# Performance work log

Measured on AMD Instinct MI355X. Metric: run time of the kernel, lower is better.

The kernel has to match this reference:

```python
import jax, jax.numpy as jnp
import numpy as np

N = 25000   # nodes
M = 150000  # edges
D = 512     # d_Embedding
H = 8       # heads
DK = 64     # per-head key dim
DV = 64     # per-head value dim


def setup_inputs() -> dict:
    key = jax.random.key(0)
    ks = jax.random.split(key, 8)
    x = jax.random.normal(ks[0], (N, D), jnp.float32)
    edge_index = jax.random.randint(ks[1], (2, M), 0, N).astype(jnp.int32)
    s_in = 1.0 / np.sqrt(D).astype(np.float32)   # fan-in scaling like nn.Linear init
    s_ff = 1.0 / np.sqrt(H * DV).astype(np.float32)
    Wk = jax.random.normal(ks[2], (D, H * DK), jnp.float32) * s_in
    Wq = jax.random.normal(ks[3], (D, H * DK), jnp.float32) * s_in
    Wv = jax.random.normal(ks[4], (D, H * DV), jnp.float32) * s_in
    Wff = jax.random.normal(ks[5], (H * DV, D), jnp.float32) * s_ff
    bk = jnp.zeros((H * DK,), jnp.float32)
    bq = jnp.zeros((H * DK,), jnp.float32)
    bv = jnp.zeros((H * DV,), jnp.float32)
    bff = jnp.zeros((D,), jnp.float32)
    return {"x": x, "edge_index": edge_index, "Wk": Wk, "bk": bk,
            "Wq": Wq, "bq": bq, "Wv": Wv, "bv": bv, "Wff": Wff, "bff": bff}


def reference(x, edge_index, Wk, bk, Wq, bq, Wv, bv, Wff, bff):
    # Q/K/V projections with per-head reshape (make_heads)
    K = (x @ Wk + bk).reshape(-1, H, DK)
    Q = (x @ Wq + bq).reshape(-1, H, DK)
    V = (x @ Wv + bv).reshape(-1, H, DV)
    senders, receivers = edge_index[0], edge_index[1]
    # edge scores: (M, H)
    att = jnp.einsum('mhd,mhd->mh', Q[receivers], K[senders]) / np.sqrt(DK).astype(np.float32)
    att = jnp.exp(att + 3.0 - att.max())  # global-max-shifted exp, as in source
    # normalize by sum of incoming strengths per receiver node (segment softmax denom)
    ssum = jax.ops.segment_sum(att, receivers, num_segments=N)  # (N, H)
    denom = ssum[receivers]
    att = jnp.where(denom == 0, 0.0, att / jnp.where(denom == 0, 1.0, denom))
    # weighted message + scatter-add aggregate: (N, H, DV)
    msg = att[..., None] * V[senders]
    agg = jax.ops.segment_sum(msg, receivers, num_segments=N)
    # aggregate_heads: Linear over concatenated heads
    return agg.reshape(-1, H * DV) @ Wff + bff
```

## Files before the change

kernel.cpp:

```cpp
#include <hip/hip_runtime.h>
#include <hip/hip_bf16.h>

#define DMODEL 512

typedef __attribute__((ext_vector_type(8))) short bf16x8;
typedef __attribute__((ext_vector_type(4))) float f32x4;

__device__ inline void gload_lds16(const void* g, void* s) {
  __builtin_amdgcn_global_load_lds((const __attribute__((address_space(1))) void*)g,
                                   (__attribute__((address_space(3))) void*)s, 16, 0, 0);
}

__device__ inline float bflo(unsigned u) {
  union { float f; unsigned u; } c; c.u = u << 16; return c.f;
}
__device__ inline float bfhi(unsigned u) {
  union { float f; unsigned u; } c; c.u = u & 0xffff0000u; return c.f;
}

template <bool OUT_BF16, int NT>
__global__ __launch_bounds__(512, 2)
void gemm_quad(const __hip_bfloat16* __restrict__ Ap,
               const __hip_bfloat16* __restrict__ Wp,
               const float* __restrict__ bias, void* __restrict__ Cv,
               int Nrows, int ncols) {
  __shared__ __align__(16) short sA[32768];
  const int tid = threadIdx.x;
  const int lane = tid & 63, w = tid >> 6;
  const int q = blockIdx.x;
  const __hip_bfloat16* Aq = Ap + (size_t)q * 32768;

#pragma unroll
  for (int i = 0; i < 8; ++i)
    gload_lds16(Aq + (size_t)(i * 512 + tid) * 8, &sA[(i * 512 + tid) * 8]);
  __syncthreads();

  const int l15 = lane & 15, lq = lane >> 4;

#pragma unroll 1
  for (int gs = 0; gs < NT / 4; ++gs) {
    const int ntb = w * NT + gs * 4;
    const __hip_bfloat16* Wb = Wp + (size_t)ntb * 16 * 512 + lane * 8;
    f32x4 acc[4][4] = {};
    bf16x8 b_cur[4], b_nxt[4];
#pragma unroll
    for (int n = 0; n < 4; ++n)
      b_cur[n] = *(const bf16x8*)(Wb + (size_t)(n * 16) * 512);

#pragma unroll 1
    for (int c = 0; c < 16; ++c) {
      if (c < 15) {
#pragma unroll
        for (int n = 0; n < 4; ++n)
          b_nxt[n] = *(const bf16x8*)(Wb + (size_t)(n * 16 + c + 1) * 512);
      }
#pragma unroll
      for (int m = 0; m < 4; ++m) {
        bf16x8 af = *(const bf16x8*)&sA[(m * 16 + c) * 512 + lane * 8];
#pragma unroll
        for (int n = 0; n < 4; ++n)
          acc[m][n] = __builtin_amdgcn_mfma_f32_16x16x32_bf16(af, b_cur[n], acc[m][n], 0, 0, 0);
      }
      if (c < 15) {
#pragma unroll
        for (int n = 0; n < 4; ++n) b_cur[n] = b_nxt[n];
      }
    }

#pragma unroll
    for (int m = 0; m < 4; ++m) {
      int rowb = q * 64 + m * 16;
#pragma unroll
      for (int n = 0; n < 4; ++n) {
        int col = (ntb + n) * 16 + l15;
        float bv = bias[col];
#pragma unroll
        for (int i = 0; i < 4; ++i) {
          int row = rowb + lq * 4 + i;
          if (row < Nrows) {
            float v = acc[m][n][i] + bv;
            if (OUT_BF16)
              ((__hip_bfloat16*)Cv)[(size_t)row * ncols + col] = __float2bfloat16(v);
            else
              ((float*)Cv)[(size_t)row * ncols + col] = v;
          }
        }
      }
    }
  }
}

__global__ void cvtp_kernel(const float* __restrict__ x, __hip_bfloat16* __restrict__ xp,
                            int Nrows, int NpadRows) {
  int tid = blockIdx.x * 256 + threadIdx.x;
  int r = tid >> 6, kb = tid & 63;
  if (r >= NpadRows) return;
  int t = r >> 4, c = kb >> 2, qq = kb & 3, lp = qq * 16 + (r & 15);
  __hip_bfloat16* dst = xp + (size_t)t * 8192 + c * 512 + lp * 8;
  union { ushort4 u[2]; __hip_bfloat16 h[8]; } o;
#pragma unroll
  for (int j = 0; j < 8; ++j) o.h[j] = __float2bfloat16(0.f);
  if (r < Nrows) {
    float4 v0 = *(const float4*)(x + (size_t)r * DMODEL + kb * 8);
    float4 v1 = *(const float4*)(x + (size_t)r * DMODEL + kb * 8 + 4);
    o.h[0] = __float2bfloat16(v0.x); o.h[1] = __float2bfloat16(v0.y);
    o.h[2] = __float2bfloat16(v0.z); o.h[3] = __float2bfloat16(v0.w);
    o.h[4] = __float2bfloat16(v1.x); o.h[5] = __float2bfloat16(v1.y);
    o.h[6] = __float2bfloat16(v1.z); o.h[7] = __float2bfloat16(v1.w);
  }
  *(ushort4*)dst = o.u[0];
  *(ushort4*)(dst + 4) = o.u[1];
}

__global__ __launch_bounds__(256)
void wp_kernel(const float* __restrict__ Wk, const float* __restrict__ Wq,
               const float* __restrict__ Wv, const float* __restrict__ Wff,
               __hip_bfloat16* __restrict__ Wp_qkv, __hip_bfloat16* __restrict__ Wp_ff) {
  int c = blockIdx.x;
  int S = blockIdx.y;
  const float* W; __hip_bfloat16* dst;
  if (S < 8)       { W = Wk;  dst = Wp_qkv + (size_t)S * 32768; }
  else if (S < 16) { W = Wq;  dst = Wp_qkv + (size_t)S * 32768; }
  else if (S < 24) { W = Wv;  dst = Wp_qkv + (size_t)S * 32768; }
  else             { W = Wff; dst = Wp_ff + (size_t)(S - 24) * 32768; }
  int colbase = (S & 7) * 64;
  __shared__ float tile[32][64];
  for (int idx = threadIdx.x; idx < 2048; idx += 256) {
    int r = idx >> 6, col = idx & 63;
    tile[r][col] = W[(size_t)(c * 32 + r) * DMODEL + colbase + col];
  }
  __syncthreads();
  int n = threadIdx.x >> 6, l = threadIdx.x & 63;
  union { ushort4 u[2]; __hip_bfloat16 h[8]; } o;
#pragma unroll
  for (int j = 0; j < 8; ++j)
    o.h[j] = __float2bfloat16(tile[(l >> 4) * 8 + j][n * 16 + (l & 15)]);
  __hip_bfloat16* p = dst + ((size_t)(n * 16 + c) * 64 + l) * 8;
  *(ushort4*)p = o.u[0];
  *(ushort4*)(p + 4) = o.u[1];
}

__global__ void bias_kernel(const float* __restrict__ bk, const float* __restrict__ bq,
                            const float* __restrict__ bv, float* __restrict__ o) {
  int i = blockIdx.x * 256 + threadIdx.x;
  if (i < 512) o[i] = bk[i];
  else if (i < 1024) o[i] = bq[i - 512];
  else if (i < 1536) o[i] = bv[i - 1024];
}

__global__ void hist_kernel(const int* __restrict__ recv, int* __restrict__ deg, int M_) {
  int m = blockIdx.x * 256 + threadIdx.x;
  if (m < M_) atomicAdd(&deg[recv[m]], 1);
}

__global__ __launch_bounds__(256)
void scan_block(const int* __restrict__ deg, int* __restrict__ offs,
                int* __restrict__ bsum, int n) {
  __shared__ int sd[256];
  const int t = threadIdx.x;
  const int base = blockIdx.x * 1024;
  int v[4], s = 0;
#pragma unroll
  for (int j = 0; j < 4; ++j) {
    int idx = base + t * 4 + j;
    v[j] = (idx < n) ? deg[idx] : 0;
    s += v[j];
  }
  sd[t] = s;
  __syncthreads();
  for (int off = 1; off < 256; off <<= 1) {
    int x = (t >= off) ? sd[t - off] : 0;
    __syncthreads();
    sd[t] += x;
    __syncthreads();
  }
  int run = sd[t] - s;
#pragma unroll
  for (int j = 0; j < 4; ++j) {
    int idx = base + t * 4 + j;
    if (idx < n) offs[idx] = run;
    run += v[j];
  }
  if (t == 255) bsum[blockIdx.x] = sd[255];
}

__global__ void scan_mid(const int* __restrict__ bsum, int* __restrict__ bbase,
                         int nb, int* __restrict__ offs, int n) {
  int t = threadIdx.x;
  int x = (t < nb) ? bsum[t] : 0;
  int v = x;
  for (int off = 1; off < 64; off <<= 1) {
    int y = __shfl_up(v, off);
    if (t >= off) v += y;
  }
  if (t < nb) bbase[t] = v - x;
  if (t == nb - 1) offs[n] = v;
}

__global__ void scan_add(int* __restrict__ offs, const int* __restrict__ bbase,
                         int* __restrict__ cursor, int n) {
  int i = blockIdx.x * 256 + threadIdx.x;
  if (i < n) {
    int o = offs[i] + bbase[i >> 10];
    offs[i] = o;
    cursor[i] = o;
  }
}

__global__ void fill_kernel(const int* __restrict__ senders, const int* __restrict__ recv,
                            int* __restrict__ cursor, int* __restrict__ sidx, int M_) {
  int m = blockIdx.x * 256 + threadIdx.x;
  if (m < M_) {
    int pos = atomicAdd(&cursor[recv[m]], 1);
    sidx[pos] = senders[m];
  }
}

__global__ __launch_bounds__(256)
void attn_kernel(const __hip_bfloat16* __restrict__ QKV, const int* __restrict__ sidx,
                 const int* __restrict__ offs, __hip_bfloat16* __restrict__ aggp, int n) {
  const int lane = threadIdx.x & 63;
  const int wid  = threadIdx.x >> 6;
  const int r = blockIdx.x * 4 + wid;
  if (r >= n) return;
  const int start = offs[r];
  const int end   = offs[r + 1];

  uint4 qr = *(const uint4*)(QKV + (size_t)r * 1536 + 512 + lane * 8);
  float q[8] = {bflo(qr.x), bfhi(qr.x), bflo(qr.y), bfhi(qr.y),
                bflo(qr.z), bfhi(qr.z), bflo(qr.w), bfhi(qr.w)};

  float ssum = 0.f;
  float acc[8] = {};
  int e = start;
  for (; e + 2 <= end; e += 2) {
    int s0 = sidx[e], s1 = sidx[e + 1];
    const __hip_bfloat16* p0 = QKV + (size_t)s0 * 1536 + lane * 8;
    const __hip_bfloat16* p1 = QKV + (size_t)s1 * 1536 + lane * 8;
    uint4 k0 = *(const uint4*)p0;
    uint4 v0 = *(const uint4*)(p0 + 1024);
    uint4 k1 = *(const uint4*)p1;
    uint4 v1 = *(const uint4*)(p1 + 1024);
    float d0 = q[0] * bflo(k0.x) + q[1] * bfhi(k0.x) + q[2] * bflo(k0.y) + q[3] * bfhi(k0.y)
             + q[4] * bflo(k0.z) + q[5] * bfhi(k0.z) + q[6] * bflo(k0.w) + q[7] * bfhi(k0.w);
    float d1 = q[0] * bflo(k1.x) + q[1] * bfhi(k1.x) + q[2] * bflo(k1.y) + q[3] * bfhi(k1.y)
             + q[4] * bflo(k1.z) + q[5] * bfhi(k1.z) + q[6] * bflo(k1.w) + q[7] * bfhi(k1.w);
    d0 += __shfl_xor(d0, 1); d1 += __shfl_xor(d1, 1);
    d0 += __shfl_xor(d0, 2); d1 += __shfl_xor(d1, 2);
    d0 += __shfl_xor(d0, 4); d1 += __shfl_xor(d1, 4);
    float w0 = expf(d0 * 0.125f), w1 = expf(d1 * 0.125f);
    ssum += w0 + w1;
    acc[0] += w0 * bflo(v0.x) + w1 * bflo(v1.x);
    acc[1] += w0 * bfhi(v0.x) + w1 * bfhi(v1.x);
    acc[2] += w0 * bflo(v0.y) + w1 * bflo(v1.y);
    acc[3] += w0 * bfhi(v0.y) + w1 * bfhi(v1.y);
    acc[4] += w0 * bflo(v0.z) + w1 * bflo(v1.z);
    acc[5] += w0 * bfhi(v0.z) + w1 * bfhi(v1.z);
    acc[6] += w0 * bflo(v0.w) + w1 * bflo(v1.w);
    acc[7] += w0 * bfhi(v0.w) + w1 * bfhi(v1.w);
  }
  if (e < end) {
    int s0 = sidx[e];
    const __hip_bfloat16* p0 = QKV + (size_t)s0 * 1536 + lane * 8;
    uint4 k0 = *(const uint4*)p0;
    uint4 v0 = *(const uint4*)(p0 + 1024);
    float d0 = q[0] * bflo(k0.x) + q[1] * bfhi(k0.x) + q[2] * bflo(k0.y) + q[3] * bfhi(k0.y)
             + q[4] * bflo(k0.z) + q[5] * bfhi(k0.z) + q[6] * bflo(k0.w) + q[7] * bfhi(k0.w);
    d0 += __shfl_xor(d0, 1);
    d0 += __shfl_xor(d0, 2);
    d0 += __shfl_xor(d0, 4);
    float w0 = expf(d0 * 0.125f);
    ssum += w0;
    acc[0] += w0 * bflo(v0.x); acc[1] += w0 * bfhi(v0.x);
    acc[2] += w0 * bflo(v0.y); acc[3] += w0 * bfhi(v0.y);
    acc[4] += w0 * bflo(v0.z); acc[5] += w0 * bfhi(v0.z);
    acc[6] += w0 * bflo(v0.w); acc[7] += w0 * bfhi(v0.w);
  }
  const float inv = (end > start) ? 1.0f / ssum : 0.f;
  union { ushort4 u[2]; __hip_bfloat16 h[8]; } o;
#pragma unroll
  for (int j = 0; j < 8; ++j) o.h[j] = __float2bfloat16(acc[j] * inv);
  int t = r >> 4, c = lane >> 2, qq = lane & 3, lp = qq * 16 + (r & 15);
  __hip_bfloat16* dst = aggp + (size_t)t * 8192 + c * 512 + lp * 8;
  *(ushort4*)dst = o.u[0];
  *(ushort4*)(dst + 4) = o.u[1];
}

extern "C" void kernel_launch(void* const* d_in, const int* in_sizes, int n_in,
                              void* d_out, int out_size, void* d_ws, size_t ws_size,
                              hipStream_t stream) {
  const float* x    = (const float*)d_in[0];
  const int*   eidx = (const int*)d_in[1];
  const float* Wk   = (const float*)d_in[2];
  const float* bk   = (const float*)d_in[3];
  const float* Wq   = (const float*)d_in[4];
  const float* bq   = (const float*)d_in[5];
  const float* Wv   = (const float*)d_in[6];
  const float* bv   = (const float*)d_in[7];
  const float* Wff  = (const float*)d_in[8];
  const float* bff  = (const float*)d_in[9];
  float* out = (float*)d_out;

  const int N_ = in_sizes[0] / DMODEL;
  const int M_ = in_sizes[1] / 2;
  const int* senders = eidx;
  const int* recv    = eidx + M_;

  const int T16 = (N_ + 15) / 16;
  const int Q4  = (T16 + 3) / 4;
  const int Npad = Q4 * 64;

  __hip_bfloat16* xp    = (__hip_bfloat16*)d_ws;
  __hip_bfloat16* QKVb  = xp + (size_t)Npad * DMODEL;
  __hip_bfloat16* aggp  = QKVb + (size_t)N_ * 1536;
  __hip_bfloat16* Wp_qkv = aggp + (size_t)Npad * DMODEL;
  __hip_bfloat16* Wp_ff  = Wp_qkv + (size_t)24 * 32768;
  float* bqkv = (float*)(Wp_ff + (size_t)8 * 32768);
  int* deg    = (int*)(bqkv + 1536);
  int* offs   = deg + N_;
  int* cursor = offs + N_ + 1;
  int* sidx   = cursor + N_;
  int* bsum   = sidx + M_;
  int* bbase  = bsum + 64;

  const int nblk = (N_ + 1023) / 1024;

  cvtp_kernel<<<(Npad * 64 + 255) / 256, 256, 0, stream>>>(x, xp, N_, Npad);
  wp_kernel<<<dim3(16, 32), 256, 0, stream>>>(Wk, Wq, Wv, Wff, Wp_qkv, Wp_ff);
  bias_kernel<<<6, 256, 0, stream>>>(bk, bq, bv, bqkv);

  hipMemsetAsync(deg, 0, N_ * sizeof(int), stream);
  hist_kernel<<<(M_ + 255) / 256, 256, 0, stream>>>(recv, deg, M_);
  scan_block<<<nblk, 256, 0, stream>>>(deg, offs, bsum, N_);
  scan_mid<<<1, 64, 0, stream>>>(bsum, bbase, nblk, offs, N_);
  scan_add<<<(N_ + 255) / 256, 256, 0, stream>>>(offs, bbase, cursor, N_);
  fill_kernel<<<(M_ + 255) / 256, 256, 0, stream>>>(senders, recv, cursor, sidx, M_);

  gemm_quad<true, 12><<<Q4, 512, 0, stream>>>(xp, Wp_qkv, bqkv, QKVb, N_, 1536);

  attn_kernel<<<(N_ + 3) / 4, 256, 0, stream>>>(QKVb, sidx, offs, aggp, N_);

  gemm_quad<false, 4><<<Q4, 512, 0, stream>>>(aggp, Wp_ff, bff, out, N_, DMODEL);
}
```

Before: 313.1 us.

## Reorder packed weight layout, stagger k/stripe order per block, raise occupancy hint

The packed weight layout is changed so that the four n-subtiles of each k-chunk sit next to each other (c*4+n), making each chunk's B loads contiguous. Each block starts at a different k-chunk offset and a different stripe order, so concurrent blocks spread their reads across weight memory instead of all hitting the same lines. The B prefetch becomes an explicit A/B ping-pong double buffer, and the launch bounds ask for 4 blocks per SIMD instead of 2. The higher occupancy target may force register spills or limit unrolling, and the pack kernel and the GEMM must stay consistent on the new layout.

```diff
diff --git a/kernel.cpp b/kernel.cpp
--- a/kernel.cpp
+++ b/kernel.cpp
@@ -19,7 +19,7 @@
 }
 
 template <bool OUT_BF16, int NT>
-__global__ __launch_bounds__(512, 2)
+__global__ __launch_bounds__(512, 4)
 void gemm_quad(const __hip_bfloat16* __restrict__ Ap,
                const __hip_bfloat16* __restrict__ Wp,
                const float* __restrict__ bias, void* __restrict__ Cv,
@@ -36,34 +36,63 @@
   __syncthreads();
 
   const int l15 = lane & 15, lq = lane >> 4;
+  const int roff = q & 15;
+  constexpr int NG = NT / 4;
 
 #pragma unroll 1
-  for (int gs = 0; gs < NT / 4; ++gs) {
+  for (int gs0 = 0; gs0 < NG; ++gs0) {
+    int gs = gs0 + (q % NG); if (gs >= NG) gs -= NG;
     const int ntb = w * NT + gs * 4;
-    const __hip_bfloat16* Wb = Wp + (size_t)ntb * 16 * 512 + lane * 8;
+    const int stripe = w * NG + gs;
+    const __hip_bfloat16* Wb = Wp + (size_t)stripe * 32768 + lane * 8;
     f32x4 acc[4][4] = {};
-    bf16x8 b_cur[4], b_nxt[4];
-#pragma unroll
-    for (int n = 0; n < 4; ++n)
-      b_cur[n] = *(const bf16x8*)(Wb + (size_t)(n * 16) * 512);
+    bf16x8 bA0, bA1, bA2, bA3, bB0, bB1, bB2, bB3;
+
+    {
+      const int cc = roff;
+      bA0 = *(const bf16x8*)(Wb + (size_t)(cc * 4 + 0) * 512);
+      bA1 = *(const bf16x8*)(Wb + (size_t)(cc * 4 + 1) * 512);
+      bA2 = *(const bf16x8*)(Wb + (size_t)(cc * 4 + 2) * 512);
+      bA3 = *(const bf16x8*)(Wb + (size_t)(cc * 4 + 3) * 512);
+    }
 
 #pragma unroll 1
-    for (int c = 0; c < 16; ++c) {
-      if (c < 15) {
-#pragma unroll
-        for (int n = 0; n < 4; ++n)
-          b_nxt[n] = *(const bf16x8*)(Wb + (size_t)(n * 16 + c + 1) * 512);
-      }
-#pragma unroll
-      for (int m = 0; m < 4; ++m) {
-        bf16x8 af = *(const bf16x8*)&sA[(m * 16 + c) * 512 + lane * 8];
-#pragma unroll
-        for (int n = 0; n < 4; ++n)
-          acc[m][n] = __builtin_amdgcn_mfma_f32_16x16x32_bf16(af, b_cur[n], acc[m][n], 0, 0, 0);
-      }
-      if (c < 15) {
-#pragma unroll
-        for (int n = 0; n < 4; ++n) b_cur[n] = b_nxt[n];
+    for (int c = 0; c < 16; c += 2) {
+      {
+        const int cc = (c + 1 + roff) & 15;
+        bB0 = *(const bf16x8*)(Wb + (size_t)(cc * 4 + 0) * 512);
+        bB1 = *(const bf16x8*)(Wb + (size_t)(cc * 4 + 1) * 512);
+        bB2 = *(const bf16x8*)(Wb + (size_t)(cc * 4 + 2) * 512);
+        bB3 = *(const bf16x8*)(Wb + (size_t)(cc * 4 + 3) * 512);
+      }
+      {
+        const int cc = (c + roff) & 15;
+#pragma unroll
+        for (int m = 0; m < 4; ++m) {
+          bf16x8 af = *(const bf16x8*)&sA[(m * 16 + cc) * 512 + lane * 8];
+          acc[m][0] = __builtin_amdgcn_mfma_f32_16x16x32_bf16(af, bA0, acc[m][0], 0, 0, 0);
+          acc[m][1] = __builtin_amdgcn_mfma_f32_16x16x32_bf16(af, bA1, acc[m][1], 0, 0, 0);
+          acc[m][2] = __builtin_amdgcn_mfma_f32_16x16x32_bf16(af, bA2, acc[m][2], 0, 0, 0);
+          acc[m][3] = __builtin_amdgcn_mfma_f32_16x16x32_bf16(af, bA3, acc[m][3], 0, 0, 0);
+        }
+      }
+      if (c + 2 < 16) {
+        const int cc = (c + 2 + roff) & 15;
+        bA0 = *(const bf16x8*)(Wb + (size_t)(cc * 4 + 0) * 512);
+        bA1 = *(const bf16x8*)(Wb + (size_t)(cc * 4 + 1) * 512);
+        bA2 = *(const bf16x8*)(Wb + (size_t)(cc * 4 + 2) * 512);
+        bA3 = *(const bf16x8*)(Wb + (size_t)(cc * 4 + 3) * 512);
+      }
+      {
+        const int cc = (c + 1 + roff) & 15;
+#pragma unroll
+        for (int m = 0; m < 4; ++m) {
+          bf16x8 af = *(const bf16x8*)&sA[(m * 16 + cc) * 512 + lane * 8];
+          acc[m][0] = __builtin_amdgcn_mfma_f32_16x16x32_bf16(af, bB0, acc[m][0], 0, 0, 0);
+          acc[m][1] = __builtin_amdgcn_mfma_f32_16x16x32_bf16(af, bB1, acc[m][1], 0, 0, 0);
+          acc[m][2] = __builtin_amdgcn_mfma_f32_16x16x32_bf16(af, bB2, acc[m][2], 0, 0, 0);
+          acc[m][3] = __builtin_amdgcn_mfma_f32_16x16x32_bf16(af, bB3, acc[m][3], 0, 0, 0);
+        }
       }
     }
 
@@ -135,7 +164,7 @@
 #pragma unroll
   for (int j = 0; j < 8; ++j)
     o.h[j] = __float2bfloat16(tile[(l >> 4) * 8 + j][n * 16 + (l & 15)]);
-  __hip_bfloat16* p = dst + ((size_t)(n * 16 + c) * 64 + l) * 8;
+  __hip_bfloat16* p = dst + ((size_t)(c * 4 + n) * 64 + l) * 8;
   *(ushort4*)p = o.u[0];
   *(ushort4*)(p + 4) = o.u[1];
 }
```

Measured after the change: 300.9 us. -3.9%, faster.
